# Kernel optimization log

Hardware: AMD Instinct MI355X
Metric: run time of the kernel (lower is better)

## Reference

```python
import jax, jax.numpy as jnp
import numpy as np

B, T, D, H, L = 32, 512, 256, 512, 3


def setup_inputs() -> dict:
    key = jax.random.key(0)
    ks = jax.random.split(key, 14)
    def lin(k, fan_in, shape):
        return jax.random.normal(k, shape, jnp.float32) / np.sqrt(fan_in)
    inp = {"x": jax.random.normal(ks[0], (B, T, D), jnp.float32)}
    dims_in = [D, H, H]
    i = 1
    for l in range(L):
        inp[f"Wi{l}"] = lin(ks[i + 0], dims_in[l], (3 * H, dims_in[l]))
        inp[f"bi{l}"] = lin(ks[i + 1], dims_in[l], (3 * H,))
        inp[f"Wh{l}"] = lin(ks[i + 2], H, (3 * H, H))
        inp[f"bh{l}"] = lin(ks[i + 3], H, (3 * H,))
        i += 4
    return inp


def _cell(Wi, bi, Wh, bh, xin, h):
    # faithful to ExponentialGatingGRUCell (h2h term appears twice in n preact)
    h2h = h @ Wh.T + bh                      # [B, 3H]
    preact = xin @ Wi.T + bi + h2h           # [B, 3H]
    g = jax.nn.sigmoid(preact[:, : 2 * H])
    r, z = g[:, :H], g[:, H:]
    r = jnp.exp(-jnp.exp(-r))
    z = jnp.exp(-jnp.exp(-z))
    n = jnp.tanh(preact[:, 2 * H:] + r * h2h[:, 2 * H:])
    return (1.0 - z) * n + z * h


def _forward(x, params):
    h0 = tuple(jnp.zeros((x.shape[0], H), x.dtype) for _ in range(L))

    def step(carry, x_t):
        hs = list(carry)
        inp = x_t
        for l in range(L):
            Wi, bi, Wh, bh = params[l]
            hs[l] = _cell(Wi, bi, Wh, bh, inp, hs[l])
            inp = hs[l]
        return tuple(hs), None

    hT, _ = jax.lax.scan(step, h0, jnp.swapaxes(x, 0, 1))  # scan over time
    return hT[-1][:, None, :]  # [B, 1, H]


def reference(x, Wi0, bi0, Wh0, bh0, Wi1, bi1, Wh1, bh1, Wi2, bi2, Wh2, bh2):
    params = [(Wi0, bi0, Wh0, bh0), (Wi1, bi1, Wh1, bh1), (Wi2, bi2, Wh2, bh2)]
    return _forward(x, params)
```

## Files before the change

kernel.cpp:

```cpp
#include <hip/hip_runtime.h>
#include <hip/hip_bf16.h>

typedef __attribute__((ext_vector_type(4))) float fx4;
typedef __attribute__((ext_vector_type(8))) short bf8;
typedef __attribute__((ext_vector_type(4))) short sx4;
typedef __attribute__((ext_vector_type(4))) int ix4;

#define NBLK 96
#define HSZ (32 * 512)

__device__ __forceinline__ short f2bf(float f) {
  __hip_bfloat16 h = __float2bfloat16(f);
  return *reinterpret_cast<short*>(&h);
}
__device__ __forceinline__ float bf2f(short s) {
  union { unsigned u; float f; } c; c.u = ((unsigned)(unsigned short)s) << 16; return c.f;
}
__device__ __forceinline__ float rcpf(float x) { return __builtin_amdgcn_rcpf(x); }
__device__ __forceinline__ bf8 asbf8(ix4 v) { union { ix4 i; bf8 b; } u; u.i = v; return u.b; }

#define LDH(dst, p, OFF) \
  asm volatile("global_load_dwordx4 %0, %1, off offset:" OFF " sc0 sc1" \
               : "=v"(dst) : "v"(p) : "memory")
#define LDP(dst, p, OFF) \
  asm volatile("global_load_dwordx4 %0, %1, off offset:" OFF \
               : "=v"(dst) : "v"(p) : "memory")
#define LD8(OP, A, P) do { \
  OP(A[0], P, "0");   OP(A[1], P, "64");  OP(A[2], P, "128"); OP(A[3], P, "192"); \
  OP(A[4], P, "256"); OP(A[5], P, "320"); OP(A[6], P, "384"); OP(A[7], P, "448"); } while (0)

__global__ __launch_bounds__(256) void conv_x_k(const float* __restrict__ x,
                                                short* __restrict__ xhi, short* __restrict__ xlo) {
  int i = blockIdx.x * 256 + threadIdx.x;
  fx4 v = *(const fx4*)(x + (size_t)i * 4);
  int k = (i * 4) & 255;
  int row = (i * 4) >> 8;
  int b = row >> 9, t = row & 511;
  sx4 hi, lo;
#pragma unroll
  for (int e = 0; e < 4; ++e) {
    hi[e] = f2bf(v[e]);
    lo[e] = f2bf(v[e] - bf2f(hi[e]));
  }
  size_t o = ((size_t)(t * 32 + b)) * 256 + k;
  *(sx4*)(xhi + o) = hi;
  *(sx4*)(xlo + o) = lo;
}

template<int L>
__device__ __forceinline__ void rec3_body(
    float (*m_lds)[32][52], float* bias_s,
    const short* __restrict__ xth, const short* __restrict__ xtl,
    const float* __restrict__ Wi, const float* __restrict__ bi,
    const float* __restrict__ Wh, const float* __restrict__ bh,
    short* __restrict__ hg, int* flags, float* __restrict__ out)
{
  const int tid = threadIdx.x;
  const int bid = blockIdx.x;
  const int j0 = (bid & 31) * 16;
  const int w = tid >> 6, lane = tid & 63, lm = lane & 15, lk = lane >> 4;
  const bool inW = (w < 2);
  constexpr int KIN = (L == 0) ? 256 : 512;

  short* hgl = hg + (size_t)L * 6 * HSZ;
  const short* hgp = (L > 0) ? (hg + (size_t)(L - 1) * 6 * HSZ) : hg;

  const int kbase = inW ? ((L == 0) ? 0 : w * 256) : (w - 2) * 256;
  const float* Wf = inW ? Wi : Wh;
  const int wstr = inW ? KIN : 512;

  bf8 bwh[3][8], bwl[3][8];
#pragma unroll
  for (int g = 0; g < 3; ++g) {
    const int grow = g * 512 + j0 + lm;
#pragma unroll
    for (int ks = 0; ks < 8; ++ks) {
      const float* src = Wf + (size_t)grow * wstr + kbase + ks * 32 + lk * 8;
      fx4 f0 = *(const fx4*)(src);
      fx4 f1 = *(const fx4*)(src + 4);
      bf8 vh, vl;
#pragma unroll
      for (int e = 0; e < 4; ++e) {
        vh[e] = f2bf(f0[e]);     vl[e] = f2bf(f0[e] - bf2f(vh[e]));
        vh[4 + e] = f2bf(f1[e]); vl[4 + e] = f2bf(f1[e] - bf2f(vh[4 + e]));
      }
      bwh[g][ks] = vh; bwl[g][ks] = vl;
    }
  }
  if (tid < 48) bias_s[tid] = bi[(tid >> 4) * 512 + j0 + (tid & 15)];
  else if (tid < 96) {
    const int u = tid - 48;
    bias_s[48 + u] = bh[(u >> 4) * 512 + j0 + (u & 15)];
  }
  {
    const int b = tid >> 3, zc = (tid & 7) * 2;
    __hip_atomic_store((int*)(hgl + (size_t)4 * HSZ + b * 512 + j0 + zc), 0,
                       __ATOMIC_RELAXED, __HIP_MEMORY_SCOPE_AGENT);
    __hip_atomic_store((int*)(hgl + (size_t)5 * HSZ + b * 512 + j0 + zc), 0,
                       __ATOMIC_RELAXED, __HIP_MEMORY_SCOPE_AGENT);
  }
  __syncthreads();
  if (tid == 0)
    __hip_atomic_store(flags + bid * 32, 2, __ATOMIC_RELAXED, __HIP_MEMORY_SCOPE_AGENT);

  constexpr int FBASE = (L == 0) ? 0 : (L - 1) * 32;
  constexpr int FCNT  = (L == 1) ? 96 : 64;
  const int cb = tid >> 3, c2 = (tid & 7) * 2;
  float hv0 = 0.f, hv1 = 0.f;
  int bufw = 0;

  for (int s = 0; s < 512; ++s) {
    ix4 rh[2][8], rl[2][8];
    if (L == 0 && inW) {
      const short* xh = xth + (size_t)(s * 32 + w * 16 + lm) * 256 + lk * 8;
      const short* xl = xtl + (size_t)(s * 32 + w * 16 + lm) * 256 + lk * 8;
      LD8(LDP, rh[0], xh);
      LD8(LDP, rl[0], xl);
    }

    if (tid < FCNT) {
      const int f = FBASE + tid;
      const int fl = f >> 5;
      const int thr = (fl < L) ? (s + 3) : ((fl == L) ? (s + 2) : s);
      while (__hip_atomic_load(flags + f * 32, __ATOMIC_RELAXED,
                               __HIP_MEMORY_SCOPE_AGENT) < thr)
        __builtin_amdgcn_s_sleep(1);
    }
    __syncthreads();

    const int bufr = (bufw == 0) ? 2 : bufw - 1;
    if (!(L == 0 && inW)) {
      const short* basep = inW ? (hgp + (size_t)(bufw * 2) * HSZ)
                               : (hgl + (size_t)(bufr * 2) * HSZ);
      const short* s0h = basep + (size_t)lm * 512 + kbase + lk * 8;
      const short* s1h = s0h + 16 * 512;
      const short* s0l = s0h + HSZ;
      const short* s1l = s1h + HSZ;
      LD8(LDH, rh[0], s0h); LD8(LDH, rh[1], s1h);
      LD8(LDH, rl[0], s0l); LD8(LDH, rl[1], s1l);
    }
    asm volatile("s_waitcnt vmcnt(0)" ::: "memory");
    __builtin_amdgcn_sched_barrier(0);

    fx4 acc[2][3];
#pragma unroll
    for (int mt = 0; mt < 2; ++mt)
#pragma unroll
      for (int g = 0; g < 3; ++g) acc[mt][g] = (fx4){0.f, 0.f, 0.f, 0.f};

    if (L == 0 && inW) {
#pragma unroll
      for (int ks = 0; ks < 8; ++ks) {
        bf8 ah = asbf8(rh[0][ks]);
        bf8 al = asbf8(rl[0][ks]);
#pragma unroll
        for (int g = 0; g < 3; ++g) {
          acc[0][g] = __builtin_amdgcn_mfma_f32_16x16x32_bf16(ah, bwh[g][ks], acc[0][g], 0, 0, 0);
          acc[0][g] = __builtin_amdgcn_mfma_f32_16x16x32_bf16(al, bwh[g][ks], acc[0][g], 0, 0, 0);
          acc[0][g] = __builtin_amdgcn_mfma_f32_16x16x32_bf16(ah, bwl[g][ks], acc[0][g], 0, 0, 0);
        }
      }
    } else {
#pragma unroll
      for (int ks = 0; ks < 8; ++ks) {
#pragma unroll
        for (int mt = 0; mt < 2; ++mt) {
          bf8 ah = asbf8(rh[mt][ks]);
          bf8 al = asbf8(rl[mt][ks]);
#pragma unroll
          for (int g = 0; g < 3; ++g) {
            acc[mt][g] = __builtin_amdgcn_mfma_f32_16x16x32_bf16(ah, bwh[g][ks], acc[mt][g], 0, 0, 0);
            acc[mt][g] = __builtin_amdgcn_mfma_f32_16x16x32_bf16(al, bwh[g][ks], acc[mt][g], 0, 0, 0);
            acc[mt][g] = __builtin_amdgcn_mfma_f32_16x16x32_bf16(ah, bwl[g][ks], acc[mt][g], 0, 0, 0);
          }
        }
      }
    }

    if (L == 0 && inW) {
#pragma unroll
      for (int g = 0; g < 3; ++g)
#pragma unroll
        for (int q = 0; q < 4; ++q)
          m_lds[0][w * 16 + lk * 4 + q][g * 16 + lm] = acc[0][g][q];
    } else {
#pragma unroll
      for (int mt = 0; mt < 2; ++mt)
#pragma unroll
        for (int g = 0; g < 3; ++g)
#pragma unroll
          for (int q = 0; q < 4; ++q)
            m_lds[w][mt * 16 + lk * 4 + q][g * 16 + lm] = acc[mt][g][q];
    }
    __syncthreads();

    float av[3][2], hh[3][2];
#pragma unroll
    for (int g = 0; g < 3; ++g)
#pragma unroll
      for (int e = 0; e < 2; ++e) {
        const int c = g * 16 + c2 + e;
        float ain = m_lds[0][cb][c];
        if (L > 0) ain += m_lds[1][cb][c];
        av[g][e] = ain + bias_s[c];
        hh[g][e] = m_lds[2][cb][c] + m_lds[3][cb][c] + bias_s[48 + c];
      }
    float hvv[2] = {hv0, hv1}, hn[2];
#pragma unroll
    for (int e = 0; e < 2; ++e) {
      float pr = av[0][e] + hh[0][e];
      float pz = av[1][e] + hh[1][e];
      float h2n = hh[2][e];
      float pn = av[2][e] + h2n;
      float sr = rcpf(1.f + __expf(-pr));
      float rr = __expf(-__expf(-sr));
      float sz = rcpf(1.f + __expf(-pz));
      float zz = __expf(-__expf(-sz));
      float na = pn + rr * h2n;
      float ex = __expf(2.f * na);
      float nn = 1.f - 2.f * rcpf(ex + 1.f);
      hn[e] = (1.f - zz) * nn + zz * hvv[e];
    }
    hv0 = hn[0]; hv1 = hn[1];
    short h0h = f2bf(hn[0]), h0l = f2bf(hn[0] - bf2f(h0h));
    short h1h = f2bf(hn[1]), h1l = f2bf(hn[1] - bf2f(h1h));
    int packh = (int)(unsigned short)h0h | ((int)(unsigned short)h1h << 16);
    int packl = (int)(unsigned short)h0l | ((int)(unsigned short)h1l << 16);

    short* hw = hgl + (size_t)(bufw * 2) * HSZ;
    __hip_atomic_store((int*)(hw + (size_t)cb * 512 + j0 + c2), packh,
                       __ATOMIC_RELAXED, __HIP_MEMORY_SCOPE_AGENT);
    __hip_atomic_store((int*)(hw + HSZ + (size_t)cb * 512 + j0 + c2), packl,
                       __ATOMIC_RELAXED, __HIP_MEMORY_SCOPE_AGENT);
    if (L == 2 && s == 511) {
      out[(size_t)cb * 512 + j0 + c2] = hn[0];
      out[(size_t)cb * 512 + j0 + c2 + 1] = hn[1];
    }
    __syncthreads();
    if (tid == 0)
      __hip_atomic_store(flags + bid * 32, s + 3,
                         __ATOMIC_RELAXED, __HIP_MEMORY_SCOPE_AGENT);

    bufw = (bufw == 2) ? 0 : bufw + 1;
  }
}

__global__ __launch_bounds__(256, 1) void rec3(
    const short* __restrict__ xth, const short* __restrict__ xtl,
    const float* __restrict__ Wi0, const float* __restrict__ bi0,
    const float* __restrict__ Wh0, const float* __restrict__ bh0,
    const float* __restrict__ Wi1, const float* __restrict__ bi1,
    const float* __restrict__ Wh1, const float* __restrict__ bh1,
    const float* __restrict__ Wi2, const float* __restrict__ bi2,
    const float* __restrict__ Wh2, const float* __restrict__ bh2,
    short* __restrict__ hg, int* flags, float* __restrict__ out)
{
  __shared__ __align__(16) float m_lds[4][32][52];
  __shared__ float bias_s[96];
  const int l = blockIdx.x >> 5;
  if (l == 0)
    rec3_body<0>(m_lds, bias_s, xth, xtl, Wi0, bi0, Wh0, bh0, hg, flags, out);
  else if (l == 1)
    rec3_body<1>(m_lds, bias_s, nullptr, nullptr, Wi1, bi1, Wh1, bh1, hg, flags, out);
  else
    rec3_body<2>(m_lds, bias_s, nullptr, nullptr, Wi2, bi2, Wh2, bh2, hg, flags, out);
}

extern "C" void kernel_launch(void* const* d_in, const int* in_sizes, int n_in,
                              void* d_out, int out_size, void* d_ws, size_t ws_size,
                              hipStream_t stream) {
  const float* x   = (const float*)d_in[0];
  const float* Wi0 = (const float*)d_in[1];
  const float* bi0 = (const float*)d_in[2];
  const float* Wh0 = (const float*)d_in[3];
  const float* bh0 = (const float*)d_in[4];
  const float* Wi1 = (const float*)d_in[5];
  const float* bi1 = (const float*)d_in[6];
  const float* Wh1 = (const float*)d_in[7];
  const float* bh1 = (const float*)d_in[8];
  const float* Wi2 = (const float*)d_in[9];
  const float* bi2 = (const float*)d_in[10];
  const float* Wh2 = (const float*)d_in[11];
  const float* bh2 = (const float*)d_in[12];
  float* out = (float*)d_out;
  (void)in_sizes; (void)n_in; (void)out_size; (void)ws_size;

  char* ws = (char*)d_ws;
  size_t off = 0;
  auto alloc = [&](size_t b) { char* p = ws + off; off = (off + b + 255) & ~(size_t)255; return p; };
  short* xth   = (short*)alloc(16384ull * 256 * 2);
  short* xtl   = (short*)alloc(16384ull * 256 * 2);
  short* hg    = (short*)alloc(3ull * 6 * HSZ * 2);
  int*   flags = (int*)alloc(NBLK * 32 * 4);

  hipMemsetAsync(flags, 0, NBLK * 32 * 4, stream);
  hipLaunchKernelGGL(conv_x_k, dim3(4096), dim3(256), 0, stream, x, xth, xtl);
  hipLaunchKernelGGL(rec3, dim3(NBLK), dim3(256), 0, stream,
                     xth, xtl,
                     Wi0, bi0, Wh0, bh0,
                     Wi1, bi1, Wh1, bh1,
                     Wi2, bi2, Wh2, bh2,
                     hg, flags, out);
}
```

Before: 3.296 ms.

## Double block to 8 waves and replace per-block flags with per-wave layer counters

```diff
diff --git a/kernel.cpp b/kernel.cpp
--- a/kernel.cpp
+++ b/kernel.cpp
@@ -25,9 +25,8 @@
 #define LDP(dst, p, OFF) \
   asm volatile("global_load_dwordx4 %0, %1, off offset:" OFF \
                : "=v"(dst) : "v"(p) : "memory")
-#define LD8(OP, A, P) do { \
-  OP(A[0], P, "0");   OP(A[1], P, "64");  OP(A[2], P, "128"); OP(A[3], P, "192"); \
-  OP(A[4], P, "256"); OP(A[5], P, "320"); OP(A[6], P, "384"); OP(A[7], P, "448"); } while (0)
+#define STSH(p, v) \
+  asm volatile("global_store_short %0, %1, off sc0 sc1" :: "v"(p), "v"(v) : "memory")
 
 __global__ __launch_bounds__(256) void conv_x_k(const float* __restrict__ x,
                                                 short* __restrict__ xhi, short* __restrict__ xlo) {
@@ -47,97 +46,137 @@
   *(sx4*)(xlo + o) = lo;
 }
 
+template<int KS>
+__device__ __forceinline__ void load_w(bf8 (&bwh)[3][4], bf8 (&bwl)[3][4],
+    const float* Wf, int wstr, int j0, int lm, int lk, int kbase) {
+#pragma unroll
+  for (int g = 0; g < 3; ++g) {
+    const int grow = g * 512 + j0 + lm;
+#pragma unroll
+    for (int ks = 0; ks < KS; ++ks) {
+      const float* src = Wf + (size_t)grow * wstr + kbase + ks * 32 + lk * 8;
+      fx4 f0 = *(const fx4*)(src);
+      fx4 f1 = *(const fx4*)(src + 4);
+      bf8 vh, vl;
+#pragma unroll
+      for (int e = 0; e < 4; ++e) {
+        vh[e] = f2bf(f0[e]);     vl[e] = f2bf(f0[e] - bf2f(vh[e]));
+        vh[4 + e] = f2bf(f1[e]); vl[4 + e] = f2bf(f1[e] - bf2f(vh[4 + e]));
+      }
+      bwh[g][ks] = vh; bwl[g][ks] = vl;
+    }
+  }
+}
+
+__device__ __forceinline__ void load_h4(ix4 (&rh)[2][4], ix4 (&rl)[2][4],
+    const short* base, int lm, int lk, int kbase) {
+  const short* p0 = base + (size_t)lm * 512 + kbase + lk * 8;
+  const short* p1 = p0 + 16 * 512;
+  const short* q0 = p0 + HSZ;
+  const short* q1 = p1 + HSZ;
+  LDH(rh[0][0], p0, "0"); LDH(rh[0][1], p0, "64"); LDH(rh[0][2], p0, "128"); LDH(rh[0][3], p0, "192");
+  LDH(rh[1][0], p1, "0"); LDH(rh[1][1], p1, "64"); LDH(rh[1][2], p1, "128"); LDH(rh[1][3], p1, "192");
+  LDH(rl[0][0], q0, "0"); LDH(rl[0][1], q0, "64"); LDH(rl[0][2], q0, "128"); LDH(rl[0][3], q0, "192");
+  LDH(rl[1][0], q1, "0"); LDH(rl[1][1], q1, "64"); LDH(rl[1][2], q1, "128"); LDH(rl[1][3], q1, "192");
+}
+
+template<int KS>
+__device__ __forceinline__ void do_mfma(fx4 (&acc)[2][3],
+    const ix4 (&rh)[2][4], const ix4 (&rl)[2][4],
+    const bf8 (&bwh)[3][4], const bf8 (&bwl)[3][4]) {
+#pragma unroll
+  for (int ks = 0; ks < KS; ++ks) {
+#pragma unroll
+    for (int mt = 0; mt < 2; ++mt) {
+      bf8 ah = asbf8(rh[mt][ks]);
+      bf8 al = asbf8(rl[mt][ks]);
+#pragma unroll
+      for (int g = 0; g < 3; ++g) {
+        acc[mt][g] = __builtin_amdgcn_mfma_f32_16x16x32_bf16(ah, bwh[g][ks], acc[mt][g], 0, 0, 0);
+        acc[mt][g] = __builtin_amdgcn_mfma_f32_16x16x32_bf16(al, bwh[g][ks], acc[mt][g], 0, 0, 0);
+        acc[mt][g] = __builtin_amdgcn_mfma_f32_16x16x32_bf16(ah, bwl[g][ks], acc[mt][g], 0, 0, 0);
+      }
+    }
+  }
+}
+
 template<int L>
 __device__ __forceinline__ void rec3_body(
     float (*m_lds)[32][52], float* bias_s,
     const short* __restrict__ xth, const short* __restrict__ xtl,
     const float* __restrict__ Wi, const float* __restrict__ bi,
     const float* __restrict__ Wh, const float* __restrict__ bh,
-    short* __restrict__ hg, int* flags, float* __restrict__ out)
+    short* __restrict__ hg, int* cnt, float* __restrict__ out)
 {
   const int tid = threadIdx.x;
   const int bid = blockIdx.x;
   const int j0 = (bid & 31) * 16;
   const int w = tid >> 6, lane = tid & 63, lm = lane & 15, lk = lane >> 4;
-  const bool inW = (w < 2);
+  const bool inW = (w < 4);
   constexpr int KIN = (L == 0) ? 256 : 512;
 
   short* hgl = hg + (size_t)L * 6 * HSZ;
   const short* hgp = (L > 0) ? (hg + (size_t)(L - 1) * 6 * HSZ) : hg;
 
-  const int kbase = inW ? ((L == 0) ? 0 : w * 256) : (w - 2) * 256;
-  const float* Wf = inW ? Wi : Wh;
-  const int wstr = inW ? KIN : 512;
-
-  bf8 bwh[3][8], bwl[3][8];
-#pragma unroll
-  for (int g = 0; g < 3; ++g) {
-    const int grow = g * 512 + j0 + lm;
-#pragma unroll
-    for (int ks = 0; ks < 8; ++ks) {
-      const float* src = Wf + (size_t)grow * wstr + kbase + ks * 32 + lk * 8;
-      fx4 f0 = *(const fx4*)(src);
-      fx4 f1 = *(const fx4*)(src + 4);
-      bf8 vh, vl;
-#pragma unroll
-      for (int e = 0; e < 4; ++e) {
-        vh[e] = f2bf(f0[e]);     vl[e] = f2bf(f0[e] - bf2f(vh[e]));
-        vh[4 + e] = f2bf(f1[e]); vl[4 + e] = f2bf(f1[e] - bf2f(vh[4 + e]));
-      }
-      bwh[g][ks] = vh; bwl[g][ks] = vl;
-    }
+  const int kbase = inW ? w * (KIN / 4) : (w - 4) * 128;
+
+  bf8 bwh[3][4], bwl[3][4];
+  if (inW) {
+    if constexpr (L == 0) load_w<2>(bwh, bwl, Wi, KIN, j0, lm, lk, kbase);
+    else                  load_w<4>(bwh, bwl, Wi, KIN, j0, lm, lk, kbase);
+  } else {
+    load_w<4>(bwh, bwl, Wh, 512, j0, lm, lk, kbase);
   }
   if (tid < 48) bias_s[tid] = bi[(tid >> 4) * 512 + j0 + (tid & 15)];
-  else if (tid < 96) {
-    const int u = tid - 48;
+  else if (tid >= 64 && tid < 112) {
+    const int u = tid - 64;
     bias_s[48 + u] = bh[(u >> 4) * 512 + j0 + (u & 15)];
   }
-  {
+  if (tid < 256) {
     const int b = tid >> 3, zc = (tid & 7) * 2;
     __hip_atomic_store((int*)(hgl + (size_t)4 * HSZ + b * 512 + j0 + zc), 0,
                        __ATOMIC_RELAXED, __HIP_MEMORY_SCOPE_AGENT);
     __hip_atomic_store((int*)(hgl + (size_t)5 * HSZ + b * 512 + j0 + zc), 0,
                        __ATOMIC_RELAXED, __HIP_MEMORY_SCOPE_AGENT);
   }
-  __syncthreads();
-  if (tid == 0)
-    __hip_atomic_store(flags + bid * 32, 2, __ATOMIC_RELAXED, __HIP_MEMORY_SCOPE_AGENT);
-
-  constexpr int FBASE = (L == 0) ? 0 : (L - 1) * 32;
-  constexpr int FCNT  = (L == 1) ? 96 : 64;
-  const int cb = tid >> 3, c2 = (tid & 7) * 2;
-  float hv0 = 0.f, hv1 = 0.f;
+  asm volatile("s_waitcnt vmcnt(0)" ::: "memory");
+  if (lane == 0)
+    __hip_atomic_fetch_add(cnt + L * 16, 1, __ATOMIC_RELAXED, __HIP_MEMORY_SCOPE_AGENT);
+
+  const int cb = tid >> 4, cc = tid & 15;
+  float hv = 0.f;
   int bufw = 0;
 
   for (int s = 0; s < 512; ++s) {
-    ix4 rh[2][8], rl[2][8];
+    ix4 rh[2][4], rl[2][4];
     if (L == 0 && inW) {
-      const short* xh = xth + (size_t)(s * 32 + w * 16 + lm) * 256 + lk * 8;
-      const short* xl = xtl + (size_t)(s * 32 + w * 16 + lm) * 256 + lk * 8;
-      LD8(LDP, rh[0], xh);
-      LD8(LDP, rl[0], xl);
-    }
-
-    if (tid < FCNT) {
-      const int f = FBASE + tid;
-      const int fl = f >> 5;
-      const int thr = (fl < L) ? (s + 3) : ((fl == L) ? (s + 2) : s);
-      while (__hip_atomic_load(flags + f * 32, __ATOMIC_RELAXED,
-                               __HIP_MEMORY_SCOPE_AGENT) < thr)
-        __builtin_amdgcn_s_sleep(1);
+      const short* x0 = xth + (size_t)(s * 32 + lm) * 256 + kbase + lk * 8;
+      const short* x1 = x0 + 16 * 256;
+      const short* y0 = xtl + (size_t)(s * 32 + lm) * 256 + kbase + lk * 8;
+      const short* y1 = y0 + 16 * 256;
+      LDP(rh[0][0], x0, "0"); LDP(rh[0][1], x0, "64");
+      LDP(rh[1][0], x1, "0"); LDP(rh[1][1], x1, "64");
+      LDP(rl[0][0], y0, "0"); LDP(rl[0][1], y0, "64");
+      LDP(rl[1][0], y1, "0"); LDP(rl[1][1], y1, "64");
+    }
+
+    if (w == 0) {
+      const int* cp = nullptr; int need = 0;
+      if (lane == 0)               { cp = cnt + L * 16;       need = 256 * (s + 1); }
+      else if (lane == 1 && L > 0) { cp = cnt + (L - 1) * 16; need = 256 * (s + 2); }
+      else if (lane == 2 && L < 2) { cp = cnt + (L + 1) * 16; need = 256 * (s - 1); }
+      if (cp)
+        while (__hip_atomic_load(cp, __ATOMIC_RELAXED, __HIP_MEMORY_SCOPE_AGENT) < need)
+          __builtin_amdgcn_s_sleep(2);
     }
     __syncthreads();
 
     const int bufr = (bufw == 0) ? 2 : bufw - 1;
-    if (!(L == 0 && inW)) {
-      const short* basep = inW ? (hgp + (size_t)(bufw * 2) * HSZ)
-                               : (hgl + (size_t)(bufr * 2) * HSZ);
-      const short* s0h = basep + (size_t)lm * 512 + kbase + lk * 8;
-      const short* s1h = s0h + 16 * 512;
-      const short* s0l = s0h + HSZ;
-      const short* s1l = s1h + HSZ;
-      LD8(LDH, rh[0], s0h); LD8(LDH, rh[1], s1h);
-      LD8(LDH, rl[0], s0l); LD8(LDH, rl[1], s1l);
+    if (inW) {
+      if constexpr (L > 0)
+        load_h4(rh, rl, hgp + (size_t)(bufw * 2) * HSZ, lm, lk, kbase);
+    } else {
+      load_h4(rh, rl, hgl + (size_t)(bufr * 2) * HSZ, lm, lk, kbase);
     }
     asm volatile("s_waitcnt vmcnt(0)" ::: "memory");
     __builtin_amdgcn_sched_barrier(0);
@@ -147,105 +186,60 @@
     for (int mt = 0; mt < 2; ++mt)
 #pragma unroll
       for (int g = 0; g < 3; ++g) acc[mt][g] = (fx4){0.f, 0.f, 0.f, 0.f};
-
-    if (L == 0 && inW) {
-#pragma unroll
-      for (int ks = 0; ks < 8; ++ks) {
-        bf8 ah = asbf8(rh[0][ks]);
-        bf8 al = asbf8(rl[0][ks]);
-#pragma unroll
-        for (int g = 0; g < 3; ++g) {
-          acc[0][g] = __builtin_amdgcn_mfma_f32_16x16x32_bf16(ah, bwh[g][ks], acc[0][g], 0, 0, 0);
-          acc[0][g] = __builtin_amdgcn_mfma_f32_16x16x32_bf16(al, bwh[g][ks], acc[0][g], 0, 0, 0);
-          acc[0][g] = __builtin_amdgcn_mfma_f32_16x16x32_bf16(ah, bwl[g][ks], acc[0][g], 0, 0, 0);
-        }
-      }
+    if (inW) {
+      if constexpr (L == 0) do_mfma<2>(acc, rh, rl, bwh, bwl);
+      else                  do_mfma<4>(acc, rh, rl, bwh, bwl);
     } else {
-#pragma unroll
-      for (int ks = 0; ks < 8; ++ks) {
-#pragma unroll
-        for (int mt = 0; mt < 2; ++mt) {
-          bf8 ah = asbf8(rh[mt][ks]);
-          bf8 al = asbf8(rl[mt][ks]);
-#pragma unroll
-          for (int g = 0; g < 3; ++g) {
-            acc[mt][g] = __builtin_amdgcn_mfma_f32_16x16x32_bf16(ah, bwh[g][ks], acc[mt][g], 0, 0, 0);
-            acc[mt][g] = __builtin_amdgcn_mfma_f32_16x16x32_bf16(al, bwh[g][ks], acc[mt][g], 0, 0, 0);
-            acc[mt][g] = __builtin_amdgcn_mfma_f32_16x16x32_bf16(ah, bwl[g][ks], acc[mt][g], 0, 0, 0);
-          }
-        }
-      }
-    }
-
-    if (L == 0 && inW) {
+      do_mfma<4>(acc, rh, rl, bwh, bwl);
+    }
+
+#pragma unroll
+    for (int mt = 0; mt < 2; ++mt)
 #pragma unroll
       for (int g = 0; g < 3; ++g)
 #pragma unroll
         for (int q = 0; q < 4; ++q)
-          m_lds[0][w * 16 + lk * 4 + q][g * 16 + lm] = acc[0][g][q];
-    } else {
-#pragma unroll
-      for (int mt = 0; mt < 2; ++mt)
-#pragma unroll
-        for (int g = 0; g < 3; ++g)
-#pragma unroll
-          for (int q = 0; q < 4; ++q)
-            m_lds[w][mt * 16 + lk * 4 + q][g * 16 + lm] = acc[mt][g][q];
-    }
+          m_lds[w][mt * 16 + lk * 4 + q][g * 16 + lm] = acc[mt][g][q];
     __syncthreads();
 
-    float av[3][2], hh[3][2];
-#pragma unroll
-    for (int g = 0; g < 3; ++g)
-#pragma unroll
-      for (int e = 0; e < 2; ++e) {
-        const int c = g * 16 + c2 + e;
-        float ain = m_lds[0][cb][c];
-        if (L > 0) ain += m_lds[1][cb][c];
-        av[g][e] = ain + bias_s[c];
-        hh[g][e] = m_lds[2][cb][c] + m_lds[3][cb][c] + bias_s[48 + c];
-      }
-    float hvv[2] = {hv0, hv1}, hn[2];
-#pragma unroll
-    for (int e = 0; e < 2; ++e) {
-      float pr = av[0][e] + hh[0][e];
-      float pz = av[1][e] + hh[1][e];
-      float h2n = hh[2][e];
-      float pn = av[2][e] + h2n;
-      float sr = rcpf(1.f + __expf(-pr));
-      float rr = __expf(-__expf(-sr));
-      float sz = rcpf(1.f + __expf(-pz));
-      float zz = __expf(-__expf(-sz));
-      float na = pn + rr * h2n;
-      float ex = __expf(2.f * na);
-      float nn = 1.f - 2.f * rcpf(ex + 1.f);
-      hn[e] = (1.f - zz) * nn + zz * hvv[e];
-    }
-    hv0 = hn[0]; hv1 = hn[1];
-    short h0h = f2bf(hn[0]), h0l = f2bf(hn[0] - bf2f(h0h));
-    short h1h = f2bf(hn[1]), h1l = f2bf(hn[1] - bf2f(h1h));
-    int packh = (int)(unsigned short)h0h | ((int)(unsigned short)h1h << 16);
-    int packl = (int)(unsigned short)h0l | ((int)(unsigned short)h1l << 16);
-
-    short* hw = hgl + (size_t)(bufw * 2) * HSZ;
-    __hip_atomic_store((int*)(hw + (size_t)cb * 512 + j0 + c2), packh,
-                       __ATOMIC_RELAXED, __HIP_MEMORY_SCOPE_AGENT);
-    __hip_atomic_store((int*)(hw + HSZ + (size_t)cb * 512 + j0 + c2), packl,
-                       __ATOMIC_RELAXED, __HIP_MEMORY_SCOPE_AGENT);
-    if (L == 2 && s == 511) {
-      out[(size_t)cb * 512 + j0 + c2] = hn[0];
-      out[(size_t)cb * 512 + j0 + c2 + 1] = hn[1];
-    }
-    __syncthreads();
-    if (tid == 0)
-      __hip_atomic_store(flags + bid * 32, s + 3,
-                         __ATOMIC_RELAXED, __HIP_MEMORY_SCOPE_AGENT);
+    float ain[3], hhv[3];
+#pragma unroll
+    for (int g = 0; g < 3; ++g) {
+      const int col = g * 16 + cc;
+      ain[g] = m_lds[0][cb][col] + m_lds[1][cb][col] + m_lds[2][cb][col] +
+               m_lds[3][cb][col] + bias_s[col];
+      hhv[g] = m_lds[4][cb][col] + m_lds[5][cb][col] + m_lds[6][cb][col] +
+               m_lds[7][cb][col] + bias_s[48 + col];
+    }
+    float pr = ain[0] + hhv[0];
+    float pz = ain[1] + hhv[1];
+    float h2n = hhv[2];
+    float pn = ain[2] + h2n;
+    float sr = rcpf(1.f + __expf(-pr));
+    float rr = __expf(-__expf(-sr));
+    float sz = rcpf(1.f + __expf(-pz));
+    float zz = __expf(-__expf(-sz));
+    float na = pn + rr * h2n;
+    float ex = __expf(2.f * na);
+    float nn = 1.f - 2.f * rcpf(ex + 1.f);
+    float hnew = (1.f - zz) * nn + zz * hv;
+    hv = hnew;
+    short hh_ = f2bf(hnew);
+    short hl_ = f2bf(hnew - bf2f(hh_));
+    short* hw = hgl + (size_t)(bufw * 2) * HSZ + (size_t)cb * 512 + j0 + cc;
+    STSH(hw, hh_);
+    STSH(hw + HSZ, hl_);
+    if (L == 2 && s == 511) out[(size_t)cb * 512 + j0 + cc] = hnew;
+
+    asm volatile("s_waitcnt vmcnt(0)" ::: "memory");
+    if (lane == 0)
+      __hip_atomic_fetch_add(cnt + L * 16, 1, __ATOMIC_RELAXED, __HIP_MEMORY_SCOPE_AGENT);
 
     bufw = (bufw == 2) ? 0 : bufw + 1;
   }
 }
 
-__global__ __launch_bounds__(256, 1) void rec3(
+__global__ __launch_bounds__(512, 1) void rec3(
     const short* __restrict__ xth, const short* __restrict__ xtl,
     const float* __restrict__ Wi0, const float* __restrict__ bi0,
     const float* __restrict__ Wh0, const float* __restrict__ bh0,
@@ -253,17 +247,17 @@
     const float* __restrict__ Wh1, const float* __restrict__ bh1,
     const float* __restrict__ Wi2, const float* __restrict__ bi2,
     const float* __restrict__ Wh2, const float* __restrict__ bh2,
-    short* __restrict__ hg, int* flags, float* __restrict__ out)
+    short* __restrict__ hg, int* cnt, float* __restrict__ out)
 {
-  __shared__ __align__(16) float m_lds[4][32][52];
+  __shared__ __align__(16) float m_lds[8][32][52];
   __shared__ float bias_s[96];
   const int l = blockIdx.x >> 5;
   if (l == 0)
-    rec3_body<0>(m_lds, bias_s, xth, xtl, Wi0, bi0, Wh0, bh0, hg, flags, out);
+    rec3_body<0>(m_lds, bias_s, xth, xtl, Wi0, bi0, Wh0, bh0, hg, cnt, out);
   else if (l == 1)
-    rec3_body<1>(m_lds, bias_s, nullptr, nullptr, Wi1, bi1, Wh1, bh1, hg, flags, out);
+    rec3_body<1>(m_lds, bias_s, nullptr, nullptr, Wi1, bi1, Wh1, bh1, hg, cnt, out);
   else
-    rec3_body<2>(m_lds, bias_s, nullptr, nullptr, Wi2, bi2, Wh2, bh2, hg, flags, out);
+    rec3_body<2>(m_lds, bias_s, nullptr, nullptr, Wi2, bi2, Wh2, bh2, hg, cnt, out);
 }
 
 extern "C" void kernel_launch(void* const* d_in, const int* in_sizes, int n_in,
@@ -291,14 +285,14 @@
   short* xth   = (short*)alloc(16384ull * 256 * 2);
   short* xtl   = (short*)alloc(16384ull * 256 * 2);
   short* hg    = (short*)alloc(3ull * 6 * HSZ * 2);
-  int*   flags = (int*)alloc(NBLK * 32 * 4);
-
-  hipMemsetAsync(flags, 0, NBLK * 32 * 4, stream);
+  int*   cnt   = (int*)alloc(3 * 16 * 4);
+
+  hipMemsetAsync(cnt, 0, 3 * 16 * 4, stream);
   hipLaunchKernelGGL(conv_x_k, dim3(4096), dim3(256), 0, stream, x, xth, xtl);
-  hipLaunchKernelGGL(rec3, dim3(NBLK), dim3(256), 0, stream,
+  hipLaunchKernelGGL(rec3, dim3(NBLK), dim3(512), 0, stream,
                      xth, xtl,
                      Wi0, bi0, Wh0, bh0,
                      Wi1, bi1, Wh1, bh1,
                      Wi2, bi2, Wh2, bh2,
-                     hg, flags, out);
-}
+                     hg, cnt, out);
+}
```

After: 6.539 ms. +98.4%, slower.

## Add per-layer aggregator blocks to replace all-to-all flag polling

Applied to the files above, without the earlier changes.

```diff
diff --git a/kernel.cpp b/kernel.cpp
--- a/kernel.cpp
+++ b/kernel.cpp
@@ -53,7 +53,7 @@
     const short* __restrict__ xth, const short* __restrict__ xtl,
     const float* __restrict__ Wi, const float* __restrict__ bi,
     const float* __restrict__ Wh, const float* __restrict__ bh,
-    short* __restrict__ hg, int* flags, float* __restrict__ out)
+    short* __restrict__ hg, int* flags, int* agg, float* __restrict__ out)
 {
   const int tid = threadIdx.x;
   const int bid = blockIdx.x;
@@ -103,8 +103,6 @@
   if (tid == 0)
     __hip_atomic_store(flags + bid * 32, 2, __ATOMIC_RELAXED, __HIP_MEMORY_SCOPE_AGENT);
 
-  constexpr int FBASE = (L == 0) ? 0 : (L - 1) * 32;
-  constexpr int FCNT  = (L == 1) ? 96 : 64;
   const int cb = tid >> 3, c2 = (tid & 7) * 2;
   float hv0 = 0.f, hv1 = 0.f;
   int bufw = 0;
@@ -118,13 +116,14 @@
       LD8(LDP, rl[0], xl);
     }
 
-    if (tid < FCNT) {
-      const int f = FBASE + tid;
-      const int fl = f >> 5;
-      const int thr = (fl < L) ? (s + 3) : ((fl == L) ? (s + 2) : s);
-      while (__hip_atomic_load(flags + f * 32, __ATOMIC_RELAXED,
-                               __HIP_MEMORY_SCOPE_AGENT) < thr)
-        __builtin_amdgcn_s_sleep(1);
+    {
+      const int* cp = nullptr; int need = 0;
+      if (tid == 0)               { cp = agg + L * 16;       need = s + 2; }
+      else if (tid == 1 && L > 0) { cp = agg + (L - 1) * 16; need = s + 3; }
+      else if (tid == 2 && L < 2) { cp = agg + (L + 1) * 16; need = s; }
+      if (cp)
+        while (__hip_atomic_load(cp, __ATOMIC_RELAXED, __HIP_MEMORY_SCOPE_AGENT) < need)
+          __builtin_amdgcn_s_sleep(1);
     }
     __syncthreads();
 
@@ -253,17 +252,36 @@
     const float* __restrict__ Wh1, const float* __restrict__ bh1,
     const float* __restrict__ Wi2, const float* __restrict__ bi2,
     const float* __restrict__ Wh2, const float* __restrict__ bh2,
-    short* __restrict__ hg, int* flags, float* __restrict__ out)
+    short* __restrict__ hg, int* flags, int* agg, float* __restrict__ out)
 {
+  const int bid = blockIdx.x;
+  if (bid >= NBLK) {
+    const int FL = bid - NBLK;
+    if (threadIdx.x >= 64) return;
+    const int lane = threadIdx.x;
+    const int* fp = flags + (FL * 32 + (lane & 31)) * 32;
+    int* ap = agg + FL * 16;
+    for (int s = -1; s < 512; ++s) {
+      const int target = s + 3;
+      while (true) {
+        int v = __hip_atomic_load(fp, __ATOMIC_RELAXED, __HIP_MEMORY_SCOPE_AGENT);
+        if (__all(v >= target)) break;
+        __builtin_amdgcn_s_sleep(1);
+      }
+      if (lane == 0)
+        __hip_atomic_store(ap, target, __ATOMIC_RELAXED, __HIP_MEMORY_SCOPE_AGENT);
+    }
+    return;
+  }
   __shared__ __align__(16) float m_lds[4][32][52];
   __shared__ float bias_s[96];
-  const int l = blockIdx.x >> 5;
+  const int l = bid >> 5;
   if (l == 0)
-    rec3_body<0>(m_lds, bias_s, xth, xtl, Wi0, bi0, Wh0, bh0, hg, flags, out);
+    rec3_body<0>(m_lds, bias_s, xth, xtl, Wi0, bi0, Wh0, bh0, hg, flags, agg, out);
   else if (l == 1)
-    rec3_body<1>(m_lds, bias_s, nullptr, nullptr, Wi1, bi1, Wh1, bh1, hg, flags, out);
+    rec3_body<1>(m_lds, bias_s, nullptr, nullptr, Wi1, bi1, Wh1, bh1, hg, flags, agg, out);
   else
-    rec3_body<2>(m_lds, bias_s, nullptr, nullptr, Wi2, bi2, Wh2, bh2, hg, flags, out);
+    rec3_body<2>(m_lds, bias_s, nullptr, nullptr, Wi2, bi2, Wh2, bh2, hg, flags, agg, out);
 }
 
 extern "C" void kernel_launch(void* const* d_in, const int* in_sizes, int n_in,
@@ -292,13 +310,15 @@
   short* xtl   = (short*)alloc(16384ull * 256 * 2);
   short* hg    = (short*)alloc(3ull * 6 * HSZ * 2);
   int*   flags = (int*)alloc(NBLK * 32 * 4);
+  int*   agg   = (int*)alloc(3 * 16 * 4);
 
   hipMemsetAsync(flags, 0, NBLK * 32 * 4, stream);
+  hipMemsetAsync(agg, 0, 3 * 16 * 4, stream);
   hipLaunchKernelGGL(conv_x_k, dim3(4096), dim3(256), 0, stream, x, xth, xtl);
-  hipLaunchKernelGGL(rec3, dim3(NBLK), dim3(256), 0, stream,
+  hipLaunchKernelGGL(rec3, dim3(NBLK + 3), dim3(256), 0, stream,
                      xth, xtl,
                      Wi0, bi0, Wh0, bh0,
                      Wi1, bi1, Wh1, bh1,
                      Wi2, bi2, Wh2, bh2,
-                     hg, flags, out);
-}
+                     hg, flags, agg, out);
+}
```

New measurement: 3.519 ms. 6.8% more time.

## Replace block-wide flag spin and barrier with per-wave ballot gating on packed flags

Applied to the files above, without the earlier changes.

```diff
diff --git a/kernel.cpp b/kernel.cpp
--- a/kernel.cpp
+++ b/kernel.cpp
@@ -28,6 +28,11 @@
 #define LD8(OP, A, P) do { \
   OP(A[0], P, "0");   OP(A[1], P, "64");  OP(A[2], P, "128"); OP(A[3], P, "192"); \
   OP(A[4], P, "256"); OP(A[5], P, "320"); OP(A[6], P, "384"); OP(A[7], P, "448"); } while (0)
+#define ST4_C(p, v) \
+  asm volatile("global_store_dword %0, %1, off sc0 sc1" :: "v"(p), "v"(v) : "memory")
+#define LD4_C(d, p) \
+  asm volatile("global_load_dword %0, %1, off sc0 sc1\n\ts_waitcnt vmcnt(0)" \
+               : "=v"(d) : "v"(p) : "memory")
 
 __global__ __launch_bounds__(256) void conv_x_k(const float* __restrict__ x,
                                                 short* __restrict__ xhi, short* __restrict__ xlo) {
@@ -47,23 +52,29 @@
   *(sx4*)(xlo + o) = lo;
 }
 
+__device__ __forceinline__ void gate_wave(const int* flags, int base, int lane, int need) {
+  const int* fp = flags + base + (lane & 31);
+  while (true) {
+    int v; LD4_C(v, fp);
+    if (__ballot(v >= need) == ~0ull) break;
+    __builtin_amdgcn_s_sleep(1);
+  }
+}
+
 template<int L>
 __device__ __forceinline__ void rec3_body(
     float (*m_lds)[32][52], float* bias_s,
     const short* __restrict__ xth, const short* __restrict__ xtl,
     const float* __restrict__ Wi, const float* __restrict__ bi,
     const float* __restrict__ Wh, const float* __restrict__ bh,
-    short* __restrict__ hg, int* flags, float* __restrict__ out)
+    short* __restrict__ hgl, const short* __restrict__ hgp,
+    int* flags, float* __restrict__ out, int p)
 {
   const int tid = threadIdx.x;
-  const int bid = blockIdx.x;
-  const int j0 = (bid & 31) * 16;
+  const int j0 = p * 16;
   const int w = tid >> 6, lane = tid & 63, lm = lane & 15, lk = lane >> 4;
   const bool inW = (w < 2);
   constexpr int KIN = (L == 0) ? 256 : 512;
-
-  short* hgl = hg + (size_t)L * 6 * HSZ;
-  const short* hgp = (L > 0) ? (hg + (size_t)(L - 1) * 6 * HSZ) : hg;
 
   const int kbase = inW ? ((L == 0) ? 0 : w * 256) : (w - 2) * 256;
   const float* Wf = inW ? Wi : Wh;
@@ -93,23 +104,20 @@
     bias_s[48 + u] = bh[(u >> 4) * 512 + j0 + (u & 15)];
   }
   {
-    const int b = tid >> 3, zc = (tid & 7) * 2;
-    __hip_atomic_store((int*)(hgl + (size_t)4 * HSZ + b * 512 + j0 + zc), 0,
-                       __ATOMIC_RELAXED, __HIP_MEMORY_SCOPE_AGENT);
-    __hip_atomic_store((int*)(hgl + (size_t)5 * HSZ + b * 512 + j0 + zc), 0,
-                       __ATOMIC_RELAXED, __HIP_MEMORY_SCOPE_AGENT);
-  }
+    const int zb = tid >> 3, zc = (tid & 7) * 2;
+    ST4_C((int*)(hgl + (size_t)4 * HSZ + (size_t)zb * 512 + j0 + zc), 0);
+    ST4_C((int*)(hgl + (size_t)5 * HSZ + (size_t)zb * 512 + j0 + zc), 0);
+  }
+  asm volatile("s_waitcnt vmcnt(0)" ::: "memory");
   __syncthreads();
-  if (tid == 0)
-    __hip_atomic_store(flags + bid * 32, 2, __ATOMIC_RELAXED, __HIP_MEMORY_SCOPE_AGENT);
-
-  constexpr int FBASE = (L == 0) ? 0 : (L - 1) * 32;
-  constexpr int FCNT  = (L == 1) ? 96 : 64;
+  if (tid == 0) ST4_C(flags + L * 32 + p, 2);
+
   const int cb = tid >> 3, c2 = (tid & 7) * 2;
   float hv0 = 0.f, hv1 = 0.f;
   int bufw = 0;
 
   for (int s = 0; s < 512; ++s) {
+    const int bufr = (bufw == 0) ? 2 : bufw - 1;
     ix4 rh[2][8], rl[2][8];
     if (L == 0 && inW) {
       const short* xh = xth + (size_t)(s * 32 + w * 16 + lm) * 256 + lk * 8;
@@ -118,26 +126,27 @@
       LD8(LDP, rl[0], xl);
     }
 
-    if (tid < FCNT) {
-      const int f = FBASE + tid;
-      const int fl = f >> 5;
-      const int thr = (fl < L) ? (s + 3) : ((fl == L) ? (s + 2) : s);
-      while (__hip_atomic_load(flags + f * 32, __ATOMIC_RELAXED,
-                               __HIP_MEMORY_SCOPE_AGENT) < thr)
-        __builtin_amdgcn_s_sleep(1);
-    }
-    __syncthreads();
-
-    const int bufr = (bufw == 0) ? 2 : bufw - 1;
-    if (!(L == 0 && inW)) {
-      const short* basep = inW ? (hgp + (size_t)(bufw * 2) * HSZ)
-                               : (hgl + (size_t)(bufr * 2) * HSZ);
-      const short* s0h = basep + (size_t)lm * 512 + kbase + lk * 8;
-      const short* s1h = s0h + 16 * 512;
-      const short* s0l = s0h + HSZ;
-      const short* s1l = s1h + HSZ;
-      LD8(LDH, rh[0], s0h); LD8(LDH, rh[1], s1h);
-      LD8(LDH, rl[0], s0l); LD8(LDH, rl[1], s1l);
+    if (!inW) {
+      gate_wave(flags, L * 32, lane, s + 2);
+    } else {
+      if (L > 0) gate_wave(flags, (L - 1) * 32, lane, s + 3);
+      if (L < 2) gate_wave(flags, (L + 1) * 32, lane, s);
+    }
+
+    if (inW) {
+      if constexpr (L > 0) {
+        const short* base = hgp + (size_t)(bufw * 2) * HSZ + (size_t)lm * 512 + kbase + lk * 8;
+        LD8(LDH, rh[0], base);
+        LD8(LDH, rh[1], base + 16 * 512);
+        LD8(LDH, rl[0], base + HSZ);
+        LD8(LDH, rl[1], base + HSZ + 16 * 512);
+      }
+    } else {
+      const short* base = hgl + (size_t)(bufr * 2) * HSZ + (size_t)lm * 512 + kbase + lk * 8;
+      LD8(LDH, rh[0], base);
+      LD8(LDH, rh[1], base + 16 * 512);
+      LD8(LDH, rl[0], base + HSZ);
+      LD8(LDH, rl[1], base + HSZ + 16 * 512);
     }
     asm volatile("s_waitcnt vmcnt(0)" ::: "memory");
     __builtin_amdgcn_sched_barrier(0);
@@ -228,18 +237,15 @@
     int packl = (int)(unsigned short)h0l | ((int)(unsigned short)h1l << 16);
 
     short* hw = hgl + (size_t)(bufw * 2) * HSZ;
-    __hip_atomic_store((int*)(hw + (size_t)cb * 512 + j0 + c2), packh,
-                       __ATOMIC_RELAXED, __HIP_MEMORY_SCOPE_AGENT);
-    __hip_atomic_store((int*)(hw + HSZ + (size_t)cb * 512 + j0 + c2), packl,
-                       __ATOMIC_RELAXED, __HIP_MEMORY_SCOPE_AGENT);
+    ST4_C((int*)(hw + (size_t)cb * 512 + j0 + c2), packh);
+    ST4_C((int*)(hw + HSZ + (size_t)cb * 512 + j0 + c2), packl);
     if (L == 2 && s == 511) {
       out[(size_t)cb * 512 + j0 + c2] = hn[0];
       out[(size_t)cb * 512 + j0 + c2 + 1] = hn[1];
     }
+    asm volatile("s_waitcnt vmcnt(0)" ::: "memory");
     __syncthreads();
-    if (tid == 0)
-      __hip_atomic_store(flags + bid * 32, s + 3,
-                         __ATOMIC_RELAXED, __HIP_MEMORY_SCOPE_AGENT);
+    if (tid == 0) ST4_C(flags + L * 32 + p, s + 3);
 
     bufw = (bufw == 2) ? 0 : bufw + 1;
   }
@@ -257,13 +263,16 @@
 {
   __shared__ __align__(16) float m_lds[4][32][52];
   __shared__ float bias_s[96];
-  const int l = blockIdx.x >> 5;
+  const int bid = blockIdx.x;
+  const int l = bid >> 5, p = bid & 31;
+  short* hgl = hg + (size_t)l * 6 * HSZ;
+  const short* hgp = (l > 0) ? (hg + (size_t)(l - 1) * 6 * HSZ) : hg;
   if (l == 0)
-    rec3_body<0>(m_lds, bias_s, xth, xtl, Wi0, bi0, Wh0, bh0, hg, flags, out);
+    rec3_body<0>(m_lds, bias_s, xth, xtl, Wi0, bi0, Wh0, bh0, hgl, hgp, flags, out, p);
   else if (l == 1)
-    rec3_body<1>(m_lds, bias_s, nullptr, nullptr, Wi1, bi1, Wh1, bh1, hg, flags, out);
+    rec3_body<1>(m_lds, bias_s, nullptr, nullptr, Wi1, bi1, Wh1, bh1, hgl, hgp, flags, out, p);
   else
-    rec3_body<2>(m_lds, bias_s, nullptr, nullptr, Wi2, bi2, Wh2, bh2, hg, flags, out);
+    rec3_body<2>(m_lds, bias_s, nullptr, nullptr, Wi2, bi2, Wh2, bh2, hgl, hgp, flags, out, p);
 }
 
 extern "C" void kernel_launch(void* const* d_in, const int* in_sizes, int n_in,
@@ -291,9 +300,9 @@
   short* xth   = (short*)alloc(16384ull * 256 * 2);
   short* xtl   = (short*)alloc(16384ull * 256 * 2);
   short* hg    = (short*)alloc(3ull * 6 * HSZ * 2);
-  int*   flags = (int*)alloc(NBLK * 32 * 4);
-
-  hipMemsetAsync(flags, 0, NBLK * 32 * 4, stream);
+  int*   flags = (int*)alloc(NBLK * 4);
+
+  hipMemsetAsync(flags, 0, NBLK * 4, stream);
   hipLaunchKernelGGL(conv_x_k, dim3(4096), dim3(256), 0, stream, x, xth, xtl);
   hipLaunchKernelGGL(rec3, dim3(NBLK), dim3(256), 0, stream,
                      xth, xtl,
```

Measured after the change: 3.829 ms. 16.2% more time.
